# Kernel optimization log

Measured on AMD Instinct MI355X. Metric: run time of the kernel, lower is better.

The kernel has to match this reference:

```python
import jax, jax.numpy as jnp
import numpy as np

N = 500000
QS = (50000, 10000)  # cardinalities of the two categorical (random-effect) inputs


def setup_inputs() -> dict:
    key = jax.random.key(0)
    ks = jax.random.split(key, 9)
    inp = {
        "X": jax.random.normal(ks[0], (N, 32), dtype=jnp.float32),
        "z0": jax.random.randint(ks[1], (N,), 0, QS[0], dtype=jnp.int32),
        "z1": jax.random.randint(ks[2], (N,), 0, QS[1], dtype=jnp.int32),
        "emb0": jax.random.normal(ks[3], (N, 16), dtype=jnp.float32),
        "emb1": jax.random.normal(ks[4], (N, 16), dtype=jnp.float32),
        "W1": jax.random.normal(ks[5], (64, 128), dtype=jnp.float32) * 0.05,
        "b1": jnp.zeros((128,), dtype=jnp.float32),
        "W2": jax.random.normal(ks[6], (128, 64), dtype=jnp.float32) * 0.05,
        "b2": jnp.zeros((64,), dtype=jnp.float32),
        "Wout": jax.random.normal(ks[7], (64, 1), dtype=jnp.float32) * 0.05,
        "bout": jnp.zeros((1,), dtype=jnp.float32),
    }
    return inp


def _seg_mean_broadcast(emb, z, q):
    # Faithful to B = divide_no_nan(Z^T @ emb, sum(Z, axis=0)); ZB = Z @ B,
    # expressed as segment-sum + count + gather (no dense one-hot matrix).
    s = jax.ops.segment_sum(emb, z, num_segments=q)                    # [q, d]
    c = jax.ops.segment_sum(jnp.ones((emb.shape[0],), emb.dtype), z,
                            num_segments=q)[:, None]                   # [q, 1]
    B = jnp.where(c > 0, s / jnp.where(c > 0, c, 1.0), 0.0)            # divide_no_nan
    return B[z]                                                        # [N, d]


def reference(X, z0, z1, emb0, emb1, W1, b1, W2, b2, Wout, bout):
    zb0 = _seg_mean_broadcast(emb0, z0, QS[0])
    zb1 = _seg_mean_broadcast(emb1, z1, QS[1])
    h = jnp.concatenate([X, zb0, zb1], axis=1)        # [N, 64]
    h = jax.nn.relu(h @ W1 + b1)                      # [N, 128]
    h = jax.nn.relu(h @ W2 + b2)                      # [N, 64]
    return h @ Wout + bout                            # [N, 1]
```

## Files before the change

### kernel.cpp

```cpp
#include <hip/hip_runtime.h>
#include <stdint.h>

#define N_ROWS 500000
#define Q0 50000
#define Q1 10000
#define NB (Q0 + Q1)
#define NTILES (N_ROWS / 16)

#define SH0T 9
#define SH1T 8
#define NP0 98
#define NP1 40
#define NPARTS (NP0 + NP1)
#define TILE_ROWS 1024
#define T_TILES ((N_ROWS + TILE_ROWS - 1) / TILE_ROWS)

#define CHUNK 2048
#define PSTRIDE (512 * 16 + 512)
#define FXS 32768.0f
#define FXSI (1.0f / 32768.0f)

typedef __attribute__((ext_vector_type(8))) short bf16x8;
typedef __attribute__((ext_vector_type(4))) float f32x4;

static __device__ __forceinline__ uint32_t f2bfu(float f) {
    uint32_t u = __builtin_bit_cast(uint32_t, f);
    u += 0x7fffu + ((u >> 16) & 1u);
    return u >> 16;
}
static __device__ __forceinline__ short f2bf(float f) { return (short)f2bfu(f); }
static __device__ __forceinline__ float bfu2f(uint32_t u) {
    return __builtin_bit_cast(float, u << 16);
}
static __device__ __forceinline__ uint32_t pk2(float x, float y) {
    return f2bfu(x) | (f2bfu(y) << 16);
}

__global__ __launch_bounds__(256) void zero_ws_kernel(uint32_t* __restrict__ p, int total) {
    int stride = gridDim.x * 256;
    for (int i = blockIdx.x * 256 + threadIdx.x; i < total; i += stride) p[i] = 0u;
}

__global__ __launch_bounds__(256) void partA_kernel(const int* __restrict__ z0,
                                                    const int* __restrict__ z1,
                                                    const float* __restrict__ emb0,
                                                    const float* __restrict__ emb1,
                                                    uint32_t* __restrict__ pid0,
                                                    uint32_t* __restrict__ pdata0,
                                                    uint32_t* __restrict__ pid1,
                                                    uint32_t* __restrict__ pdata1,
                                                    int* __restrict__ curs,
                                                    int* __restrict__ ovfcnt,
                                                    float* __restrict__ ovf,
                                                    int cap0, int cap1) {
    const bool is0 = blockIdx.x < T_TILES;
    const int tile = is0 ? blockIdx.x : blockIdx.x - T_TILES;
    const int* z = is0 ? z0 : z1;
    const float* emb = is0 ? emb0 : emb1;
    const int nparts = is0 ? NP0 : NP1;
    const int SH = is0 ? SH0T : SH1T;
    const int cap = is0 ? cap0 : cap1;
    uint32_t* pid = is0 ? pid0 : pid1;
    uint32_t* pdata = is0 ? pdata0 : pdata1;
    int* cur = curs + (is0 ? 0 : NP0);
    const int wofs = is0 ? 0 : Q0;

    __shared__ int lcnt[NP0];
    __shared__ int loff[NP0 + 1];
    __shared__ int gbase[NP0];
    __shared__ uint32_t sid[TILE_ROWS];
    __shared__ uint32_t spay[TILE_ROWS * 8];

    const int t = threadIdx.x;
    for (int i = t; i < nparts; i += 256) lcnt[i] = 0;
    __syncthreads();

    int bks[4], rnk[4];
    const int base = tile * TILE_ROWS;
#pragma unroll
    for (int i = 0; i < 4; i++) {
        int r = base + i * 256 + t;
        if (r < N_ROWS) {
            int b = z[r];
            bks[i] = b;
            rnk[i] = atomicAdd(&lcnt[b >> SH], 1);
        } else {
            bks[i] = -1;
            rnk[i] = 0;
        }
    }
    __syncthreads();
    if (t == 0) {
        int s = 0;
        for (int p = 0; p < nparts; p++) { loff[p] = s; s += lcnt[p]; }
        loff[nparts] = s;
    }
    __syncthreads();
    if (t < nparts) gbase[t] = atomicAdd(&cur[t], lcnt[t]);
    __syncthreads();

#pragma unroll
    for (int i = 0; i < 4; i++) {
        if (bks[i] < 0) continue;
        int r = base + i * 256 + t;
        int p = bks[i] >> SH;
        int s = loff[p] + rnk[i];
        sid[s] = (uint32_t)bks[i];
        const float4* e = (const float4*)(emb + (size_t)r * 16);
        float4 A = e[0], B = e[1], C = e[2], D = e[3];
        uint32_t* d = &spay[s * 8];
        d[0] = pk2(A.x, A.y); d[1] = pk2(A.z, A.w);
        d[2] = pk2(B.x, B.y); d[3] = pk2(B.z, B.w);
        d[4] = pk2(C.x, C.y); d[5] = pk2(C.z, C.w);
        d[6] = pk2(D.x, D.y); d[7] = pk2(D.z, D.w);
    }
    __syncthreads();

    const int E = loff[nparts];
    for (int s = t; s < E; s += 256) {
        int b = (int)sid[s];
        int p = b >> SH;
        int dest = gbase[p] + (s - loff[p]);
        if (dest < cap) pid[(size_t)p * cap + dest] = (uint32_t)b;
        else atomicAdd(&ovfcnt[b + wofs], 1);
    }
    for (int j = t; j < E * 8; j += 256) {
        int s = j >> 3, q = j & 7;
        int b = (int)sid[s];
        int p = b >> SH;
        int dest = gbase[p] + (s - loff[p]);
        uint32_t x = spay[j];
        if (dest < cap) {
            pdata[((size_t)p * cap + dest) * 8 + q] = x;
        } else {
            atomicAdd(&ovf[(size_t)(b + wofs) * 16 + q * 2],     bfu2f(x & 0xffffu));
            atomicAdd(&ovf[(size_t)(b + wofs) * 16 + q * 2 + 1], bfu2f(x >> 16));
        }
    }
}

__global__ __launch_bounds__(256) void partB_kernel(const uint32_t* __restrict__ pid0,
                                                    const uint32_t* __restrict__ pdata0,
                                                    const uint32_t* __restrict__ pid1,
                                                    const uint32_t* __restrict__ pdata1,
                                                    const int* __restrict__ curs,
                                                    float* __restrict__ partials,
                                                    int cap0, int cap1,
                                                    int nc0, int nc1) {
    const int bid = blockIdx.x;
    const bool is0 = bid < NP0 * nc0;
    int lp, ck;
    if (is0) { lp = bid / nc0; ck = bid % nc0; }
    else     { int r = bid - NP0 * nc0; lp = r / nc1; ck = r % nc1; }
    const int SH = is0 ? SH0T : SH1T;
    const int NBK = 1 << SH;
    const int p = is0 ? lp : NP0 + lp;
    const int cap = is0 ? cap0 : cap1;
    const uint32_t* pi = (is0 ? pid0 : pid1) + (size_t)lp * cap;
    const uint32_t* pd = (is0 ? pdata0 : pdata1) + (size_t)lp * cap * 8;
    int n = curs[p];
    if (n > cap) n = cap;
    const int start = ck * CHUNK;
    if (start >= n) return;
    const int nslots = ((start + CHUNK < n) ? CHUNK : (n - start));
    const int fb = lp << SH;

    __shared__ int sums[512 * 16];
    __shared__ int cnt[512];
    const int t = threadIdx.x;
    for (int i = t; i < NBK * 16; i += 256) sums[i] = 0;
    for (int i = t; i < NBK; i += 256) cnt[i] = 0;
    __syncthreads();

    const int half = t & 1;
    const int sbase = t >> 1;

#pragma unroll
    for (int mg = 0; mg < 2; mg++) {
        uint4 pay[8]; int lbs[8]; bool val[8];
#pragma unroll
        for (int gi = 0; gi < 8; gi++) {
            int slot = (mg * 8 + gi) * 128 + sbase;
            bool v = slot < nslots;
            val[gi] = v;
            if (v) {
                pay[gi] = *(const uint4*)(pd + (size_t)(start + slot) * 8 + half * 4);
                lbs[gi] = (int)pi[start + slot] - fb;
            }
        }
#pragma unroll
        for (int gi = 0; gi < 8; gi++) {
            if (!val[gi]) continue;
            int lb = lbs[gi];
            int* S = &sums[lb * 16];
            int d0 = half * 8;
            uint32_t xs[4] = {pay[gi].x, pay[gi].y, pay[gi].z, pay[gi].w};
#pragma unroll
            for (int jj = 0; jj < 4; jj++) {
                int da = d0 + jj * 2, db = da + 1;
                int fa = __float2int_rn(bfu2f(xs[jj] & 0xffffu) * FXS);
                int fbv = __float2int_rn(bfu2f(xs[jj] >> 16) * FXS);
                atomicAdd(S + ((da + lb) & 15), fa);
                atomicAdd(S + ((db + lb) & 15), fbv);
            }
            if (half == 0) atomicAdd(&cnt[lb], 1);
        }
    }
    __syncthreads();

    float* P = partials + (size_t)bid * PSTRIDE;
    for (int i = t; i < NBK * 16; i += 256) {
        int lb = i >> 4, d = i & 15;
        P[i] = (float)sums[lb * 16 + ((d + lb) & 15)] * FXSI;
    }
    for (int i = t; i < NBK; i += 256) P[512 * 16 + i] = (float)cnt[i];
}

__global__ __launch_bounds__(256) void combine_kernel(const float* __restrict__ partials,
                                                      const int* __restrict__ curs,
                                                      const int* __restrict__ ovfcnt,
                                                      const float* __restrict__ ovf,
                                                      uint32_t* __restrict__ meansb,
                                                      int cap0, int cap1,
                                                      int nc0, int nc1) {
    int i = blockIdx.x * 256 + threadIdx.x;
    if (i >= NB * 8) return;
    int w = i >> 3, dp = i & 7;
    int d0 = dp * 2, d1 = d0 + 1;
    const bool is0 = w < Q0;
    const int b = is0 ? w : w - Q0;
    const int lp = b >> (is0 ? SH0T : SH1T);
    const int lb = b & (is0 ? 511 : 255);
    const int p = is0 ? lp : NP0 + lp;
    const int pb = is0 ? lp * nc0 : NP0 * nc0 + lp * nc1;
    const int cap = is0 ? cap0 : cap1;
    int n = curs[p];
    if (n > cap) n = cap;
    const int nc = (n + CHUNK - 1) / CHUNK;
    float s0 = 0.0f, s1 = 0.0f, cc = 0.0f;
    for (int k = 0; k < nc; k++) {
        const float* P = partials + (size_t)(pb + k) * PSTRIDE;
        s0 += P[lb * 16 + d0];
        s1 += P[lb * 16 + d1];
        cc += P[512 * 16 + lb];
    }
    s0 += ovf[(size_t)w * 16 + d0];
    s1 += ovf[(size_t)w * 16 + d1];
    cc += (float)ovfcnt[w];
    float inv = (cc > 0.0f) ? (1.0f / cc) : 0.0f;
    meansb[(size_t)w * 8 + dp] = pk2(s0 * inv, s1 * inv);
}

__global__ __launch_bounds__(256, 2) void mlp_mfma_kernel(
    const float* __restrict__ X, const int* __restrict__ z0, const int* __restrict__ z1,
    const uint32_t* __restrict__ meansb,
    const float* __restrict__ W1, const float* __restrict__ b1,
    const float* __restrict__ W2, const float* __restrict__ b2,
    const float* __restrict__ Wout, const float* __restrict__ bout,
    float* __restrict__ out)
{
    const int lane = threadIdx.x & 63;
    const int wv = threadIdx.x >> 6;
    const int c = lane & 15;
    const int g = lane >> 4;
    const int gg = g * 8;

    bf16x8 w1f[8][2];
#pragma unroll
    for (int ct = 0; ct < 8; ct++)
#pragma unroll
        for (int ks = 0; ks < 2; ks++)
#pragma unroll
            for (int e = 0; e < 8; e++)
                w1f[ct][ks][e] = f2bf(W1[(ks * 32 + gg + e) * 128 + ct * 16 + c]);

    bf16x8 w2f[4][4];
#pragma unroll
    for (int ct = 0; ct < 4; ct++)
#pragma unroll
        for (int ks = 0; ks < 4; ks++)
#pragma unroll
            for (int e = 0; e < 8; e++) {
                int h = 16 * (2 * ks + (e >> 2)) + g * 4 + (e & 3);
                w2f[ct][ks][e] = f2bf(W2[h * 64 + ct * 16 + c]);
            }

    f32x4 b1q[8];
#pragma unroll
    for (int ct = 0; ct < 8; ct++)
        b1q[ct] = *(const f32x4*)(b1 + ct * 16 + g * 4);

    float b2v[4], wo[4];
#pragma unroll
    for (int ct = 0; ct < 4; ct++) b2v[ct] = b2[ct * 16 + c];
#pragma unroll
    for (int t = 0; t < 4; t++) wo[t] = Wout[t * 16 + c];
    const float bo = bout[0];

    const bool is0 = (gg < 16);
    const int* zp = is0 ? z0 : z1;
    const uint32_t* mb = meansb + (is0 ? 0 : (size_t)Q0 * 8);
    const int moffd = (g & 1) * 4;

    const int wave_id = blockIdx.x * 4 + wv;
    const int nw = gridDim.x * 4;
    if (wave_id >= NTILES) return;

#define XPTR(t_) ((const float4*)(X + ((size_t)(t_) * 16 + c) * 32 + gg))

    int tile = wave_id;
    float4 xa0 = XPTR(tile)[0], xa1 = XPTR(tile)[1];
    int aA = zp[tile * 16 + c];
    uint4 mA = *(const uint4*)(mb + (size_t)aA * 8 + moffd);
    const int t1i = tile + nw;
    int aB = zp[((t1i < NTILES) ? t1i : tile) * 16 + c];

    for (; tile < NTILES; tile += nw) {
        const int t1 = tile + nw;
        const int t1c = (t1 < NTILES) ? t1 : tile;
        const int t2 = tile + 2 * nw;
        const int t2c = (t2 < NTILES) ? t2 : t1c;

        float4 xb0 = XPTR(t1c)[0], xb1 = XPTR(t1c)[1];
        uint4 mB = *(const uint4*)(mb + (size_t)aB * 8 + moffd);
        int aC = zp[t2c * 16 + c];

        bf16x8 a1[2];
        a1[0][0] = f2bf(xa0.x); a1[0][1] = f2bf(xa0.y);
        a1[0][2] = f2bf(xa0.z); a1[0][3] = f2bf(xa0.w);
        a1[0][4] = f2bf(xa1.x); a1[0][5] = f2bf(xa1.y);
        a1[0][6] = f2bf(xa1.z); a1[0][7] = f2bf(xa1.w);
        a1[1] = __builtin_bit_cast(bf16x8, mA);

        f32x4 d1p[8];
#pragma unroll
        for (int ct = 0; ct < 8; ct++) {
            f32x4 acc = b1q[ct];
            acc = __builtin_amdgcn_mfma_f32_16x16x32_bf16(w1f[ct][0], a1[0], acc, 0, 0, 0);
            acc = __builtin_amdgcn_mfma_f32_16x16x32_bf16(w1f[ct][1], a1[1], acc, 0, 0, 0);
            d1p[ct] = acc;
        }

        bf16x8 a2[4];
#pragma unroll
        for (int ks = 0; ks < 4; ks++)
#pragma unroll
            for (int e = 0; e < 8; e++)
                a2[ks][e] = f2bf(fmaxf(d1p[2 * ks + (e >> 2)][e & 3], 0.0f));

        f32x4 d2[4];
#pragma unroll
        for (int ct = 0; ct < 4; ct++) {
            f32x4 acc = {b2v[ct], b2v[ct], b2v[ct], b2v[ct]};
#pragma unroll
            for (int ks = 0; ks < 4; ks++)
                acc = __builtin_amdgcn_mfma_f32_16x16x32_bf16(a2[ks], w2f[ct][ks], acc, 0, 0, 0);
            d2[ct] = acc;
        }

        float sr[4];
#pragma unroll
        for (int r = 0; r < 4; r++) {
            float s = 0.0f;
#pragma unroll
            for (int ct = 0; ct < 4; ct++)
                s = fmaf(fmaxf(d2[ct][r], 0.0f), wo[ct], s);
            sr[r] = s;
        }
#pragma unroll
        for (int m = 1; m <= 8; m <<= 1)
#pragma unroll
            for (int r = 0; r < 4; r++)
                sr[r] += __shfl_xor(sr[r], m);
        if (c == 0) {
            float4 o = {sr[0] + bo, sr[1] + bo, sr[2] + bo, sr[3] + bo};
            *(float4*)(out + tile * 16 + g * 4) = o;
        }

        xa0 = xb0; xa1 = xb1; mA = mB; aB = aC;
    }
#undef XPTR
}

extern "C" void kernel_launch(void* const* d_in, const int* in_sizes, int n_in,
                              void* d_out, int out_size, void* d_ws, size_t ws_size,
                              hipStream_t stream) {
    const float* X    = (const float*)d_in[0];
    const int*   z0   = (const int*)d_in[1];
    const int*   z1   = (const int*)d_in[2];
    const float* emb0 = (const float*)d_in[3];
    const float* emb1 = (const float*)d_in[4];
    const float* W1   = (const float*)d_in[5];
    const float* b1   = (const float*)d_in[6];
    const float* W2   = (const float*)d_in[7];
    const float* b2   = (const float*)d_in[8];
    const float* Wout = (const float*)d_in[9];
    const float* bout = (const float*)d_in[10];
    float* out = (float*)d_out;
    char* ws = (char*)d_ws;

    const size_t fixedB = (size_t)NPARTS * 4 + (size_t)NB * 4 + (size_t)NB * 64
                        + (size_t)NB * 32;
    const int c0s[4] = {6656, 5632, 5376, 0};
    const int c1s[4] = {14336, 13056, 12800, 0};
    int CAP0 = 0, CAP1 = 0, NC0 = 0, NC1 = 0, NBLK = 0;
    for (int i = 0; i < 4; i++) {
        int nc0 = (c0s[i] + CHUNK - 1) / CHUNK;
        int nc1 = (c1s[i] + CHUNK - 1) / CHUNK;
        int nblk = NP0 * nc0 + NP1 * nc1;
        size_t need = ((size_t)NP0 * c0s[i] + (size_t)NP1 * c1s[i]) * 36
                    + (size_t)nblk * PSTRIDE * 4 + fixedB;
        if (need <= ws_size) { CAP0 = c0s[i]; CAP1 = c1s[i]; NC0 = nc0; NC1 = nc1; NBLK = nblk; break; }
    }

    char* p = ws;
    uint32_t* pdata0 = (uint32_t*)p;  p += (size_t)NP0 * CAP0 * 32;
    uint32_t* pdata1 = (uint32_t*)p;  p += (size_t)NP1 * CAP1 * 32;
    uint32_t* pid0   = (uint32_t*)p;  p += (size_t)NP0 * CAP0 * 4;
    uint32_t* pid1   = (uint32_t*)p;  p += (size_t)NP1 * CAP1 * 4;
    float* partials  = (float*)p;     p += (size_t)NBLK * PSTRIDE * 4;
    uint32_t* zbase  = (uint32_t*)p;
    int* curs        = (int*)p;       p += (size_t)NPARTS * 4;
    int* ovfcnt      = (int*)p;       p += (size_t)NB * 4;
    float* ovf       = (float*)p;     p += (size_t)NB * 64;
    uint32_t* meansb = (uint32_t*)p;

    const int zero_dwords = NPARTS + NB + NB * 16;
    zero_ws_kernel<<<1024, 256, 0, stream>>>(zbase, zero_dwords);
    partA_kernel<<<2 * T_TILES, 256, 0, stream>>>(z0, z1, emb0, emb1,
                                                  pid0, pdata0, pid1, pdata1,
                                                  curs, ovfcnt, ovf, CAP0, CAP1);
    if (NBLK > 0) {
        partB_kernel<<<NBLK, 256, 0, stream>>>(pid0, pdata0, pid1, pdata1,
                                               curs, partials, CAP0, CAP1, NC0, NC1);
        combine_kernel<<<(NB * 8 + 255) / 256, 256, 0, stream>>>(partials, curs, ovfcnt,
                                                                 ovf, meansb, CAP0, CAP1,
                                                                 NC0, NC1);
    } else {
        combine_kernel<<<(NB * 8 + 255) / 256, 256, 0, stream>>>(partials, curs, ovfcnt,
                                                                 ovf, meansb, 0, 0, 0, 0);
    }
    mlp_mfma_kernel<<<1024, 256, 0, stream>>>(X, z0, z1, meansb, W1, b1, W2, b2,
                                              Wout, bout, out);
}
```

Baseline: 101.5 us.

## Stage MLP weight fragments in LDS and interleave layers to raise occupancy

Moves the bf16 W1/W2 MFMA fragments out of per-thread registers into shared memory, filled cooperatively by the four waves, and reads them from LDS inside the row loop. Layer-1 and layer-2 MFMAs are interleaved per k-slice so fewer layer-1 accumulators are live at once. Launch bounds rise from 2 to 4 blocks per SIMD. The aim is to cut VGPR pressure so more waves can hide the gather and X load latency, at the cost of extra LDS reads per tile and a block-wide barrier. An empty asm barrier on the LDS offset stops the compiler from hoisting the LDS loads back into registers.

```diff
diff --git a/kernel.cpp b/kernel.cpp
--- a/kernel.cpp
+++ b/kernel.cpp
@@ -251,7 +251,7 @@
     meansb[(size_t)w * 8 + dp] = pk2(s0 * inv, s1 * inv);
 }
 
-__global__ __launch_bounds__(256, 2) void mlp_mfma_kernel(
+__global__ __launch_bounds__(256, 4) void mlp_mfma_kernel(
     const float* __restrict__ X, const int* __restrict__ z0, const int* __restrict__ z1,
     const uint32_t* __restrict__ meansb,
     const float* __restrict__ W1, const float* __restrict__ b1,
@@ -259,31 +259,37 @@
     const float* __restrict__ Wout, const float* __restrict__ bout,
     float* __restrict__ out)
 {
+    __shared__ uint4 wl1[16][64];
+    __shared__ uint4 wl2[16][64];
+
     const int lane = threadIdx.x & 63;
     const int wv = threadIdx.x >> 6;
     const int c = lane & 15;
     const int g = lane >> 4;
     const int gg = g * 8;
 
-    bf16x8 w1f[8][2];
-#pragma unroll
-    for (int ct = 0; ct < 8; ct++)
-#pragma unroll
-        for (int ks = 0; ks < 2; ks++)
+    if (wv < 2) {
+        for (int f = wv * 8; f < wv * 8 + 8; f++) {
+            int ct = f >> 1, ks = f & 1;
+            bf16x8 fr;
 #pragma unroll
             for (int e = 0; e < 8; e++)
-                w1f[ct][ks][e] = f2bf(W1[(ks * 32 + gg + e) * 128 + ct * 16 + c]);
-
-    bf16x8 w2f[4][4];
-#pragma unroll
-    for (int ct = 0; ct < 4; ct++)
-#pragma unroll
-        for (int ks = 0; ks < 4; ks++)
+                fr[e] = f2bf(W1[(ks * 32 + gg + e) * 128 + ct * 16 + c]);
+            wl1[f][lane] = __builtin_bit_cast(uint4, fr);
+        }
+    } else {
+        for (int f = (wv - 2) * 8; f < (wv - 2) * 8 + 8; f++) {
+            int ct = f >> 2, ks = f & 3;
+            bf16x8 fr;
 #pragma unroll
             for (int e = 0; e < 8; e++) {
                 int h = 16 * (2 * ks + (e >> 2)) + g * 4 + (e & 3);
-                w2f[ct][ks][e] = f2bf(W2[h * 64 + ct * 16 + c]);
+                fr[e] = f2bf(W2[h * 64 + ct * 16 + c]);
             }
+            wl2[f][lane] = __builtin_bit_cast(uint4, fr);
+        }
+    }
+    __syncthreads();
 
     f32x4 b1q[8];
 #pragma unroll
@@ -315,7 +321,12 @@
     const int t1i = tile + nw;
     int aB = zp[((t1i < NTILES) ? t1i : tile) * 16 + c];
 
+    int zoff = 0;
     for (; tile < NTILES; tile += nw) {
+        asm volatile("" : "+v"(zoff));
+        const uint4* W1L = &wl1[0][0] + zoff;
+        const uint4* W2L = &wl2[0][0] + zoff;
+
         const int t1 = tile + nw;
         const int t1c = (t1 < NTILES) ? t1 : tile;
         const int t2 = tile + 2 * nw;
@@ -332,30 +343,37 @@
         a1[0][6] = f2bf(xa1.z); a1[0][7] = f2bf(xa1.w);
         a1[1] = __builtin_bit_cast(bf16x8, mA);
 
-        f32x4 d1p[8];
-#pragma unroll
-        for (int ct = 0; ct < 8; ct++) {
-            f32x4 acc = b1q[ct];
-            acc = __builtin_amdgcn_mfma_f32_16x16x32_bf16(w1f[ct][0], a1[0], acc, 0, 0, 0);
-            acc = __builtin_amdgcn_mfma_f32_16x16x32_bf16(w1f[ct][1], a1[1], acc, 0, 0, 0);
-            d1p[ct] = acc;
-        }
-
-        bf16x8 a2[4];
-#pragma unroll
-        for (int ks = 0; ks < 4; ks++)
+        f32x4 d2[4];
+#pragma unroll
+        for (int ct = 0; ct < 4; ct++) {
+            f32x4 v = {b2v[ct], b2v[ct], b2v[ct], b2v[ct]};
+            d2[ct] = v;
+        }
+
+#pragma unroll
+        for (int ks2 = 0; ks2 < 4; ks2++) {
+            const int cta = 2 * ks2, ctb = cta + 1;
+            f32x4 aa = b1q[cta];
+            aa = __builtin_amdgcn_mfma_f32_16x16x32_bf16(
+                     __builtin_bit_cast(bf16x8, W1L[(cta * 2 + 0) * 64 + lane]), a1[0], aa, 0, 0, 0);
+            aa = __builtin_amdgcn_mfma_f32_16x16x32_bf16(
+                     __builtin_bit_cast(bf16x8, W1L[(cta * 2 + 1) * 64 + lane]), a1[1], aa, 0, 0, 0);
+            f32x4 ab = b1q[ctb];
+            ab = __builtin_amdgcn_mfma_f32_16x16x32_bf16(
+                     __builtin_bit_cast(bf16x8, W1L[(ctb * 2 + 0) * 64 + lane]), a1[0], ab, 0, 0, 0);
+            ab = __builtin_amdgcn_mfma_f32_16x16x32_bf16(
+                     __builtin_bit_cast(bf16x8, W1L[(ctb * 2 + 1) * 64 + lane]), a1[1], ab, 0, 0, 0);
+
+            bf16x8 a2v;
 #pragma unroll
             for (int e = 0; e < 8; e++)
-                a2[ks][e] = f2bf(fmaxf(d1p[2 * ks + (e >> 2)][e & 3], 0.0f));
-
-        f32x4 d2[4];
-#pragma unroll
-        for (int ct = 0; ct < 4; ct++) {
-            f32x4 acc = {b2v[ct], b2v[ct], b2v[ct], b2v[ct]};
-#pragma unroll
-            for (int ks = 0; ks < 4; ks++)
-                acc = __builtin_amdgcn_mfma_f32_16x16x32_bf16(a2[ks], w2f[ct][ks], acc, 0, 0, 0);
-            d2[ct] = acc;
+                a2v[e] = f2bf(fmaxf(((e < 4) ? aa : ab)[e & 3], 0.0f));
+
+#pragma unroll
+            for (int ct2 = 0; ct2 < 4; ct2++)
+                d2[ct2] = __builtin_amdgcn_mfma_f32_16x16x32_bf16(
+                              a2v, __builtin_bit_cast(bf16x8, W2L[(ct2 * 4 + ks2) * 64 + lane]),
+                              d2[ct2], 0, 0, 0);
         }
 
         float sr[4];
```

New measurement: 93.13 us. 1.09x faster.
